# Kernel optimization log

Hardware: AMD Instinct MI355X
Metric: run time of the kernel (lower is better)

## Reference

```python
import jax, jax.numpy as jnp
import numpy as np

B, N, D, H = 2, 2048, 512, 8
HD = D // H
EPS = 1e-5


def layernorm(x, g, b):
    m = jnp.mean(x, axis=-1, keepdims=True)
    v = jnp.var(x, axis=-1, keepdims=True)
    return (x - m) * jax.lax.rsqrt(v + EPS) * g + b


def setup_inputs() -> dict:
    key = jax.random.key(0)
    ks = jax.random.split(key, 16)
    s = 1.0 / np.sqrt(D)
    def lin(k, din, dout):
        k1, k2 = jax.random.split(k)
        return (jax.random.uniform(k1, (din, dout), jnp.float32, -s, s),
                jax.random.uniform(k2, (dout,), jnp.float32, -s, s))
    Wq, bq = lin(ks[0], D, D)
    Wk, bk = lin(ks[1], D, D)
    Wv, bv = lin(ks[2], D, D)
    Wo, bo = lin(ks[3], D, D)
    W1, b1 = lin(ks[4], D, 2 * D)
    W2, b2 = lin(ks[5], 2 * D, D)
    return {
        'y': jax.random.normal(ks[6], (B, N, D), jnp.float32),
        'Wq': Wq, 'bq': bq, 'Wk': Wk, 'bk': bk, 'Wv': Wv, 'bv': bv,
        'Wo': Wo, 'bo': bo,
        'ln1_g': jnp.ones((D,)), 'ln1_b': jnp.zeros((D,)),
        'ln2_g': jnp.ones((D,)), 'ln2_b': jnp.zeros((D,)),
        'W1': W1, 'b1': b1, 'W2': W2, 'b2': b2,
    }


def reference(y, Wq, bq, Wk, bk, Wv, bv, Wo, bo, ln1_g, ln1_b, ln2_g, ln2_b, W1, b1, W2, b2):
    x = layernorm(y, ln1_g, ln1_b)
    def heads(W, b):
        return (x @ W + b).reshape(B, N, H, HD).transpose(0, 2, 1, 3)  # bhnc
    q = heads(Wq, bq)
    k = heads(Wk, bk)
    v = heads(Wv, bv)
    score = jax.nn.softmax(jnp.einsum('bhic,bhjc->bhij', q, k) / np.sqrt(HD), axis=-1)
    r = jnp.einsum('bhij,bhjc->bhic', score, v)
    r = r.transpose(0, 2, 1, 3).reshape(B, N, D) @ Wo + bo
    y = y + r
    h = layernorm(y, ln2_g, ln2_b)
    h = jax.nn.gelu(h @ W1 + b1, approximate=False) @ W2 + b2
    return y + h
```

## Files before the change

kernel.cpp:

```cpp
#include <hip/hip_runtime.h>

#define DEVI __device__ __forceinline__

typedef unsigned short u16;
typedef unsigned int   u32;
typedef unsigned long long u64;
typedef float  f32x4  __attribute__((ext_vector_type(4)));
typedef __bf16 bf16x8 __attribute__((ext_vector_type(8)));

union FragU { bf16x8 b; u64 u[2]; __bf16 e[8]; };

DEVI u16 f2b(float x) { __bf16 t = (__bf16)x; return __builtin_bit_cast(u16, t); }

DEVI float exp2a(float x) { float r; asm("v_exp_f32 %0, %1" : "=v"(r) : "v"(x)); return r; }

DEVI void gload16(const void* g, void* l) {
  __builtin_amdgcn_global_load_lds((const __attribute__((address_space(1))) u32*)g,
                                   (__attribute__((address_space(3))) u32*)l, 16, 0, 0);
}

DEVI int swzo(int row, int kb) {
  return ((((kb >> 4) ^ row) & 7) << 4) | ((kb ^ row) & 8) | (kb & 7);
}

DEVI u64 ldswz(const char* base, int row, int kb) {
  return *reinterpret_cast<const u64*>(base + row * 128 + swzo(row, kb));
}

DEVI size_t gaddr(int row, int kbyte, int rowbytes) {
  return (size_t)row * rowbytes + (size_t)((kbyte & ~127) + swzo(row, kbyte & 127));
}

__global__ __launch_bounds__(256)
void transpose_all(const float* __restrict__ Wq, const float* __restrict__ Wk,
                   const float* __restrict__ Wv, const float* __restrict__ Wo,
                   const float* __restrict__ W1, const float* __restrict__ W2,
                   u16* __restrict__ wqkvT, u16* __restrict__ woT,
                   u16* __restrict__ w1T, u16* __restrict__ w2T) {
  __shared__ float tile[32][33];
  const int id = blockIdx.x;
  const float* src; u16* dst; int K, N, bx, by;
  if (id < 1024) {
    const int m = id >> 8, t = id & 255;
    K = 512; N = 512; bx = t & 15; by = t >> 4;
    src = (m == 0) ? Wq : (m == 1) ? Wk : (m == 2) ? Wv : Wo;
    dst = (m == 3) ? woT : wqkvT + m * 512 * 512;
  } else if (id < 1536) {
    const int t = id - 1024; K = 512; N = 1024; bx = t & 31; by = t >> 5;
    src = W1; dst = w1T;
  } else {
    const int t = id - 1536; K = 1024; N = 512; bx = t & 15; by = t >> 4;
    src = W2; dst = w2T;
  }
  const int tx = threadIdx.x & 31, ty = threadIdx.x >> 5;
#pragma unroll
  for (int i = 0; i < 4; ++i)
    tile[ty + i * 8][tx] = src[(size_t)(by * 32 + ty + i * 8) * N + bx * 32 + tx];
  __syncthreads();
#pragma unroll
  for (int i = 0; i < 4; ++i) {
    const int n = bx * 32 + ty + i * 8;
    const int k = by * 32 + tx;
    *(u16*)((char*)dst + gaddr(n, 2 * k, 2 * K)) = f2b(tile[tx][ty + i * 8]);
  }
}

__global__ __launch_bounds__(256)
void ln_bf16(const float* __restrict__ x, const float* __restrict__ g,
             const float* __restrict__ b, char* __restrict__ out) {
  const int row = blockIdx.x;
  const int t = threadIdx.x;
  const float2 v = ((const float2*)(x + (size_t)row * 512))[t];
  float s1 = v.x + v.y, s2 = v.x * v.x + v.y * v.y;
#pragma unroll
  for (int off = 32; off; off >>= 1) { s1 += __shfl_xor(s1, off); s2 += __shfl_xor(s2, off); }
  __shared__ float a1[4], a2[4];
  const int w = t >> 6;
  if ((t & 63) == 0) { a1[w] = s1; a2[w] = s2; }
  __syncthreads();
  s1 = a1[0] + a1[1] + a1[2] + a1[3];
  s2 = a2[0] + a2[1] + a2[2] + a2[3];
  const float mean = s1 * (1.f / 512.f);
  const float var = s2 * (1.f / 512.f) - mean * mean;
  const float rstd = rsqrtf(var + 1e-5f);
  const float2 gg = ((const float2*)g)[t];
  const float2 bb = ((const float2*)b)[t];
  const u16 o0 = f2b((v.x - mean) * rstd * gg.x + bb.x);
  const u16 o1 = f2b((v.y - mean) * rstd * gg.y + bb.y);
  *(u32*)(out + gaddr(row, 4 * t, 1024)) = (u32)o0 | ((u32)o1 << 16);
}

enum { EPI_QKV = 0, EPI_RES = 1, EPI_GELU = 2 };

template <int EPI>
__global__ __launch_bounds__(256)
void gemm_bf16(const char* __restrict__ A, const char* __restrict__ Bt, int N, int K,
               const float* __restrict__ bias,
               const float* __restrict__ bq, const float* __restrict__ bk,
               const float* __restrict__ bv,
               const float* __restrict__ res, float* __restrict__ outF,
               char* __restrict__ outB,
               u16* __restrict__ qo, char* __restrict__ ko, char* __restrict__ vo) {
  __shared__ __align__(16) char sA[2][8192];
  __shared__ __align__(16) char sB[2][8192];
  const int tid = threadIdx.x;
  const int l = tid & 63, w = tid >> 6;
  const int tm = blockIdx.x, tn = blockIdx.y;
  const int wr = w >> 1, wc = w & 1;
  const int u = l >> 4, r16 = l & 15;
  const int lrow = l >> 3, lgr = l & 7;
  f32x4 acc[2][2] = {};
  const size_t KB = (size_t)K * 2;
  const char* Ab = A + (size_t)(tm * 64) * KB;
  const char* Bb = Bt + (size_t)(tn * 64) * KB;
  const int nkt = K >> 6;
  auto stage = [&](int buf, int kt) {
#pragma unroll
    for (int c = 0; c < 2; ++c) {
      const int chunk = w * 2 + c;
      const size_t off = (size_t)(chunk * 8 + lrow) * KB + (size_t)kt * 128 + (lgr << 4);
      gload16(Ab + off, sA[buf] + chunk * 1024);
      gload16(Bb + off, sB[buf] + chunk * 1024);
    }
  };
  stage(0, 0);
  int cur = 0;
  for (int kt = 0; kt < nkt; ++kt) {
    __syncthreads();
    if (kt + 1 < nkt) stage(cur ^ 1, kt + 1);
    __builtin_amdgcn_s_setprio(1);
#pragma unroll
    for (int ks = 0; ks < 2; ++ks) {
      FragU af[2], bfr[2];
      const int kb = ks * 64 + (u << 3);
#pragma unroll
      for (int i = 0; i < 2; ++i) {
        af[i].u[0]  = ldswz(sA[cur], wr * 32 + i * 16 + r16, kb);
        af[i].u[1]  = ldswz(sA[cur], wr * 32 + i * 16 + r16, kb + 32);
        bfr[i].u[0] = ldswz(sB[cur], wc * 32 + i * 16 + r16, kb);
        bfr[i].u[1] = ldswz(sB[cur], wc * 32 + i * 16 + r16, kb + 32);
      }
#pragma unroll
      for (int mi = 0; mi < 2; ++mi)
#pragma unroll
        for (int ni = 0; ni < 2; ++ni)
          acc[mi][ni] = __builtin_amdgcn_mfma_f32_16x16x32_bf16(af[mi].b, bfr[ni].b,
                                                                acc[mi][ni], 0, 0, 0);
    }
    __builtin_amdgcn_s_setprio(0);
    cur ^= 1;
  }
  const int row0 = tm * 64 + wr * 32 + (u << 2);
  const int col0 = tn * 64 + wc * 32 + r16;
#pragma unroll
  for (int mi = 0; mi < 2; ++mi) {
#pragma unroll
    for (int ni = 0; ni < 2; ++ni) {
      const int col = col0 + ni * 16;
      if (EPI == EPI_RES) {
#pragma unroll
        for (int r = 0; r < 4; ++r) {
          const int row = row0 + mi * 16 + r;
          outF[(size_t)row * N + col] = acc[mi][ni][r] + bias[col] + res[(size_t)row * N + col];
        }
      } else if (EPI == EPI_GELU) {
#pragma unroll
        for (int r = 0; r < 4; ++r) {
          const int row = row0 + mi * 16 + r;
          const float x = acc[mi][ni][r] + bias[col];
          *(u16*)(outB + gaddr(row, 2 * col, 2 * N)) =
              f2b(0.5f * x * (1.f + erff(x * 0.70710678118f)));
        }
      } else {
        const int which = col >> 9, cc = col & 511;
        const int h = cc >> 6, hd = cc & 63;
        if (which == 2) {
          const int rowa = row0 + mi * 16;
          const int bb2 = rowa >> 11, nt0 = rowa & 2047;
          const int bh = bb2 * 8 + h;
          const float bvv = bv[cc];
          union { ushort4 s; u64 q; } pk;
          pk.s.x = f2b(acc[mi][ni][0] + bvv);
          pk.s.y = f2b(acc[mi][ni][1] + bvv);
          pk.s.z = f2b(acc[mi][ni][2] + bvv);
          pk.s.w = f2b(acc[mi][ni][3] + bvv);
          *(u64*)(vo + (size_t)bh * 262144 + (size_t)(nt0 >> 6) * 8192 +
                  gaddr(hd, 2 * (nt0 & 63), 128)) = pk.q;
        } else {
#pragma unroll
          for (int r = 0; r < 4; ++r) {
            const int row = row0 + mi * 16 + r;
            const int bb2 = row >> 11, nt = row & 2047;
            const int bh = bb2 * 8 + h;
            if (which == 0)
              qo[((size_t)bh * 2048 + nt) * 64 + hd] = f2b((acc[mi][ni][r] + bq[cc]) * 0.18033688f);
            else
              *(u16*)(ko + (size_t)bh * 262144 + (size_t)(nt >> 6) * 8192 +
                      gaddr(nt & 63, 2 * hd, 128)) = f2b(acc[mi][ni][r] + bk[cc]);
          }
        }
      }
    }
  }
}

__global__ __launch_bounds__(512)
void attn_k(const u16* __restrict__ q, const char* __restrict__ kswz,
            const char* __restrict__ vswz, char* __restrict__ r_out) {
  __shared__ __align__(16) char sK[2][2][8192];
  __shared__ __align__(16) char sV[2][2][8192];
  const int tid = threadIdx.x;
  const int l = tid & 63, w = tid >> 6;
  const int kvh = w & 1, qw = w >> 1;
  const int bh = blockIdx.x, qt = blockIdx.y;
  const int u = l >> 4, r16 = l & 15;
  const char* kp = kswz + (size_t)bh * 262144;
  const char* vp = vswz + (size_t)bh * 262144;
  const int c0 = qw * 2;
  auto stage = [&](int buf, int t) {
#pragma unroll
    for (int c = 0; c < 2; ++c) {
      gload16(kp + (size_t)t * 8192 + (c0 + c) * 1024 + l * 16, sK[kvh][buf] + (c0 + c) * 1024);
      gload16(vp + (size_t)t * 8192 + (c0 + c) * 1024 + l * 16, sV[kvh][buf] + (c0 + c) * 1024);
    }
  };
  stage(0, kvh * 16);
  FragU qf[2];
  {
    const u16* qr = q + (size_t)bh * (2048 * 64) + (size_t)(qt * 64 + qw * 16 + r16) * 64 + (u << 2);
    qf[0].u[0] = *(const u64*)qr;        qf[0].u[1] = *(const u64*)(qr + 16);
    qf[1].u[0] = *(const u64*)(qr + 32); qf[1].u[1] = *(const u64*)(qr + 48);
  }
  float mrun = -1e30f, lrun = 0.f;
  f32x4 o[4] = {};
  int cur = 0;
  for (int i = 0; i < 16; ++i) {
    __syncthreads();
    if (i < 15) stage(cur ^ 1, kvh * 16 + i + 1);
    f32x4 st[4] = {};
    __builtin_amdgcn_s_setprio(1);
#pragma unroll
    for (int ks = 0; ks < 2; ++ks) {
      const int kb = ks * 64 + (u << 3);
#pragma unroll
      for (int mi = 0; mi < 4; ++mi) {
        FragU kf;
        kf.u[0] = ldswz(sK[kvh][cur], mi * 16 + r16, kb);
        kf.u[1] = ldswz(sK[kvh][cur], mi * 16 + r16, kb + 32);
        st[mi] = __builtin_amdgcn_mfma_f32_16x16x32_bf16(kf.b, qf[ks].b, st[mi], 0, 0, 0);
      }
    }
    __builtin_amdgcn_s_setprio(0);
    float tmax = -1e30f;
#pragma unroll
    for (int mi = 0; mi < 4; ++mi)
#pragma unroll
      for (int r = 0; r < 4; ++r) tmax = fmaxf(tmax, st[mi][r]);
    tmax = fmaxf(tmax, __shfl_xor(tmax, 16));
    tmax = fmaxf(tmax, __shfl_xor(tmax, 32));
    if (!__all(tmax <= mrun + 11.5f)) {
      const float mnew = fmaxf(mrun, tmax);
      const float alpha = exp2a(mrun - mnew);
      lrun *= alpha;
#pragma unroll
      for (int mo = 0; mo < 4; ++mo) o[mo] *= alpha;
      mrun = mnew;
    }
    float p[4][4];
    float tsum = 0.f;
#pragma unroll
    for (int mi = 0; mi < 4; ++mi)
#pragma unroll
      for (int r = 0; r < 4; ++r) { p[mi][r] = exp2a(st[mi][r] - mrun); tsum += p[mi][r]; }
    tsum += __shfl_xor(tsum, 16);
    tsum += __shfl_xor(tsum, 32);
    lrun += tsum;
    FragU pb[2];
#pragma unroll
    for (int ks = 0; ks < 2; ++ks)
#pragma unroll
      for (int j = 0; j < 4; ++j) {
        pb[ks].e[j]     = (__bf16)p[2 * ks][j];
        pb[ks].e[j + 4] = (__bf16)p[2 * ks + 1][j];
      }
    __builtin_amdgcn_s_setprio(1);
#pragma unroll
    for (int ks = 0; ks < 2; ++ks) {
      const int kb = ks * 64 + (u << 3);
#pragma unroll
      for (int mo = 0; mo < 4; ++mo) {
        FragU vf;
        vf.u[0] = ldswz(sV[kvh][cur], mo * 16 + r16, kb);
        vf.u[1] = ldswz(sV[kvh][cur], mo * 16 + r16, kb + 32);
        o[mo] = __builtin_amdgcn_mfma_f32_16x16x32_bf16(vf.b, pb[ks].b, o[mo], 0, 0, 0);
      }
    }
    __builtin_amdgcn_s_setprio(0);
    cur ^= 1;
  }
  __syncthreads();
  float* scrO  = (float*)&sK[0][0][0];
  float* scrML = (float*)&sV[0][0][0];
  if (kvh == 1) {
    if (u == 0) { scrML[qw * 32 + r16] = mrun; scrML[qw * 32 + 16 + r16] = lrun; }
#pragma unroll
    for (int mo = 0; mo < 4; ++mo)
#pragma unroll
      for (int r = 0; r < 4; ++r)
        scrO[qw * 1024 + (mo * 16 + u * 4 + r) * 16 + r16] = o[mo][r];
  }
  __syncthreads();
  if (kvh == 0) {
    const float m1 = scrML[qw * 32 + r16], l1 = scrML[qw * 32 + 16 + r16];
    const float m = fmaxf(mrun, m1);
    const float a0 = exp2a(mrun - m), a1 = exp2a(m1 - m);
    const float linv = 1.f / (lrun * a0 + l1 * a1);
    const float f0 = a0 * linv, f1 = a1 * linv;
    const int tok = (bh >> 3) * 2048 + qt * 64 + qw * 16 + r16;
    const int h = bh & 7;
#pragma unroll
    for (int mo = 0; mo < 4; ++mo) {
      union { ushort4 s; u64 qq; } pk;
      float vv[4];
#pragma unroll
      for (int r = 0; r < 4; ++r)
        vv[r] = o[mo][r] * f0 + scrO[qw * 1024 + (mo * 16 + u * 4 + r) * 16 + r16] * f1;
      pk.s.x = f2b(vv[0]); pk.s.y = f2b(vv[1]); pk.s.z = f2b(vv[2]); pk.s.w = f2b(vv[3]);
      *(u64*)(r_out + (size_t)tok * 1024 + h * 128 + swzo(tok, mo * 32 + (u << 3))) = pk.qq;
    }
  }
}

extern "C" void kernel_launch(void* const* d_in, const int* in_sizes, int n_in,
                              void* d_out, int out_size, void* d_ws, size_t ws_size,
                              hipStream_t stream) {
  const float* y    = (const float*)d_in[0];
  const float* Wq   = (const float*)d_in[1];
  const float* bq   = (const float*)d_in[2];
  const float* Wk   = (const float*)d_in[3];
  const float* bk   = (const float*)d_in[4];
  const float* Wv   = (const float*)d_in[5];
  const float* bv   = (const float*)d_in[6];
  const float* Wo   = (const float*)d_in[7];
  const float* bo   = (const float*)d_in[8];
  const float* ln1g = (const float*)d_in[9];
  const float* ln1b = (const float*)d_in[10];
  const float* ln2g = (const float*)d_in[11];
  const float* ln2b = (const float*)d_in[12];
  const float* W1   = (const float*)d_in[13];
  const float* b1   = (const float*)d_in[14];
  const float* W2   = (const float*)d_in[15];
  const float* b2   = (const float*)d_in[16];
  float* out = (float*)d_out;
  char* ws = (char*)d_ws;
  char* xb    = ws;
  u16*  qb    = (u16*)(ws + (4u << 20));
  char* kswz  = ws + (8u << 20);
  char* vswz  = ws + (12u << 20);
  char* rb    = ws + (16u << 20);
  char* g1b   = ws + (20u << 20);
  u16* wqkvT  = (u16*)(ws + (28u << 20));
  u16* woT    = wqkvT + 1536 * 512;
  u16* w1T    = woT + 512 * 512;
  u16* w2T    = w1T + 1024 * 512;

  transpose_all<<<2048, 256, 0, stream>>>(Wq, Wk, Wv, Wo, W1, W2, wqkvT, woT, w1T, w2T);
  ln_bf16<<<4096, 256, 0, stream>>>(y, ln1g, ln1b, xb);
  gemm_bf16<EPI_QKV><<<dim3(64, 24), 256, 0, stream>>>(
      xb, (const char*)wqkvT, 1536, 512, nullptr, bq, bk, bv,
      nullptr, nullptr, nullptr, qb, kswz, vswz);
  attn_k<<<dim3(16, 32), 512, 0, stream>>>(qb, kswz, vswz, rb);
  gemm_bf16<EPI_RES><<<dim3(64, 8), 256, 0, stream>>>(
      rb, (const char*)woT, 512, 512, bo, nullptr, nullptr, nullptr,
      y, out, nullptr, nullptr, nullptr, nullptr);
  ln_bf16<<<4096, 256, 0, stream>>>(out, ln2g, ln2b, xb);
  gemm_bf16<EPI_GELU><<<dim3(64, 16), 256, 0, stream>>>(
      xb, (const char*)w1T, 1024, 512, b1, nullptr, nullptr, nullptr,
      nullptr, nullptr, g1b, nullptr, nullptr, nullptr);
  gemm_bf16<EPI_RES><<<dim3(64, 8), 256, 0, stream>>>(
      g1b, (const char*)w2T, 512, 1024, b2, nullptr, nullptr, nullptr,
      out, out, nullptr, nullptr, nullptr, nullptr);
}
```

Measured before the change: 111.5 us.

## Enlarge GEMM tiles to 64x64 per wave and fuse weight transpose with first layernorm

The GEMM kernel is templated on the warp grid, and each wave now computes a 64x64 output tile with 4x4 MFMA fragments instead of 32x32. This gives blocks of 128x128 or 64x128, raising data reuse per LDS load and cutting block counts. The weight transpose and the first layernorm are merged into a single launch to save one kernel launch. The larger register footprint may lower occupancy, and the smaller grids (e.g. 256 blocks for the output projections) may underfill the 256 CUs.

```diff
diff --git a/kernel.cpp b/kernel.cpp
--- a/kernel.cpp
+++ b/kernel.cpp
@@ -32,36 +32,61 @@
 }
 
 __global__ __launch_bounds__(256)
-void transpose_all(const float* __restrict__ Wq, const float* __restrict__ Wk,
-                   const float* __restrict__ Wv, const float* __restrict__ Wo,
-                   const float* __restrict__ W1, const float* __restrict__ W2,
-                   u16* __restrict__ wqkvT, u16* __restrict__ woT,
-                   u16* __restrict__ w1T, u16* __restrict__ w2T) {
-  __shared__ float tile[32][33];
+void prep(const float* __restrict__ Wq, const float* __restrict__ Wk,
+          const float* __restrict__ Wv, const float* __restrict__ Wo,
+          const float* __restrict__ W1, const float* __restrict__ W2,
+          u16* __restrict__ wqkvT, u16* __restrict__ woT,
+          u16* __restrict__ w1T, u16* __restrict__ w2T,
+          const float* __restrict__ y, const float* __restrict__ ln1g,
+          const float* __restrict__ ln1b, char* __restrict__ xb) {
   const int id = blockIdx.x;
-  const float* src; u16* dst; int K, N, bx, by;
-  if (id < 1024) {
-    const int m = id >> 8, t = id & 255;
-    K = 512; N = 512; bx = t & 15; by = t >> 4;
-    src = (m == 0) ? Wq : (m == 1) ? Wk : (m == 2) ? Wv : Wo;
-    dst = (m == 3) ? woT : wqkvT + m * 512 * 512;
-  } else if (id < 1536) {
-    const int t = id - 1024; K = 512; N = 1024; bx = t & 31; by = t >> 5;
-    src = W1; dst = w1T;
+  if (id < 2048) {
+    __shared__ float tile[32][33];
+    const float* src; u16* dst; int K, N, bx, by;
+    if (id < 1024) {
+      const int m = id >> 8, t = id & 255;
+      K = 512; N = 512; bx = t & 15; by = t >> 4;
+      src = (m == 0) ? Wq : (m == 1) ? Wk : (m == 2) ? Wv : Wo;
+      dst = (m == 3) ? woT : wqkvT + m * 512 * 512;
+    } else if (id < 1536) {
+      const int t = id - 1024; K = 512; N = 1024; bx = t & 31; by = t >> 5;
+      src = W1; dst = w1T;
+    } else {
+      const int t = id - 1536; K = 1024; N = 512; bx = t & 15; by = t >> 4;
+      src = W2; dst = w2T;
+    }
+    const int tx = threadIdx.x & 31, ty = threadIdx.x >> 5;
+#pragma unroll
+    for (int i = 0; i < 4; ++i)
+      tile[ty + i * 8][tx] = src[(size_t)(by * 32 + ty + i * 8) * N + bx * 32 + tx];
+    __syncthreads();
+#pragma unroll
+    for (int i = 0; i < 4; ++i) {
+      const int n = bx * 32 + ty + i * 8;
+      const int k = by * 32 + tx;
+      *(u16*)((char*)dst + gaddr(n, 2 * k, 2 * K)) = f2b(tile[tx][ty + i * 8]);
+    }
   } else {
-    const int t = id - 1536; K = 1024; N = 512; bx = t & 15; by = t >> 4;
-    src = W2; dst = w2T;
-  }
-  const int tx = threadIdx.x & 31, ty = threadIdx.x >> 5;
-#pragma unroll
-  for (int i = 0; i < 4; ++i)
-    tile[ty + i * 8][tx] = src[(size_t)(by * 32 + ty + i * 8) * N + bx * 32 + tx];
-  __syncthreads();
-#pragma unroll
-  for (int i = 0; i < 4; ++i) {
-    const int n = bx * 32 + ty + i * 8;
-    const int k = by * 32 + tx;
-    *(u16*)((char*)dst + gaddr(n, 2 * k, 2 * K)) = f2b(tile[tx][ty + i * 8]);
+    const int row = id - 2048;
+    const int t = threadIdx.x;
+    const float2 v = ((const float2*)(y + (size_t)row * 512))[t];
+    float s1 = v.x + v.y, s2 = v.x * v.x + v.y * v.y;
+#pragma unroll
+    for (int off = 32; off; off >>= 1) { s1 += __shfl_xor(s1, off); s2 += __shfl_xor(s2, off); }
+    __shared__ float a1[4], a2[4];
+    const int w = t >> 6;
+    if ((t & 63) == 0) { a1[w] = s1; a2[w] = s2; }
+    __syncthreads();
+    s1 = a1[0] + a1[1] + a1[2] + a1[3];
+    s2 = a2[0] + a2[1] + a2[2] + a2[3];
+    const float mean = s1 * (1.f / 512.f);
+    const float var = s2 * (1.f / 512.f) - mean * mean;
+    const float rstd = rsqrtf(var + 1e-5f);
+    const float2 gg = ((const float2*)ln1g)[t];
+    const float2 bb = ((const float2*)ln1b)[t];
+    const u16 o0 = f2b((v.x - mean) * rstd * gg.x + bb.x);
+    const u16 o1 = f2b((v.y - mean) * rstd * gg.y + bb.y);
+    *(u32*)(xb + gaddr(row, 4 * t, 1024)) = (u32)o0 | ((u32)o1 << 16);
   }
 }
 
@@ -92,8 +117,8 @@
 
 enum { EPI_QKV = 0, EPI_RES = 1, EPI_GELU = 2 };
 
-template <int EPI>
-__global__ __launch_bounds__(256)
+template <int EPI, int WM, int WN>
+__global__ __launch_bounds__(WM * WN * 64)
 void gemm_bf16(const char* __restrict__ A, const char* __restrict__ Bt, int N, int K,
                const float* __restrict__ bias,
                const float* __restrict__ bq, const float* __restrict__ bk,
@@ -101,26 +126,32 @@
                const float* __restrict__ res, float* __restrict__ outF,
                char* __restrict__ outB,
                u16* __restrict__ qo, char* __restrict__ ko, char* __restrict__ vo) {
-  __shared__ __align__(16) char sA[2][8192];
-  __shared__ __align__(16) char sB[2][8192];
+  constexpr int NW = WM * WN, TM = WM * 64, TN = WN * 64;
+  constexpr int NCH = (WM + WN) * 8;
+  __shared__ __align__(16) char sA[2][TM * 128];
+  __shared__ __align__(16) char sB[2][TN * 128];
   const int tid = threadIdx.x;
   const int l = tid & 63, w = tid >> 6;
   const int tm = blockIdx.x, tn = blockIdx.y;
-  const int wr = w >> 1, wc = w & 1;
+  const int wr = w / WN, wc = w % WN;
   const int u = l >> 4, r16 = l & 15;
   const int lrow = l >> 3, lgr = l & 7;
-  f32x4 acc[2][2] = {};
+  f32x4 acc[4][4] = {};
   const size_t KB = (size_t)K * 2;
-  const char* Ab = A + (size_t)(tm * 64) * KB;
-  const char* Bb = Bt + (size_t)(tn * 64) * KB;
+  const char* Ab = A + (size_t)(tm * TM) * KB;
+  const char* Bb = Bt + (size_t)(tn * TN) * KB;
   const int nkt = K >> 6;
   auto stage = [&](int buf, int kt) {
 #pragma unroll
-    for (int c = 0; c < 2; ++c) {
-      const int chunk = w * 2 + c;
-      const size_t off = (size_t)(chunk * 8 + lrow) * KB + (size_t)kt * 128 + (lgr << 4);
-      gload16(Ab + off, sA[buf] + chunk * 1024);
-      gload16(Bb + off, sB[buf] + chunk * 1024);
+    for (int c = w; c < NCH; c += NW) {
+      if (c < WM * 8) {
+        gload16(Ab + (size_t)(c * 8 + lrow) * KB + (size_t)kt * 128 + (lgr << 4),
+                sA[buf] + c * 1024);
+      } else {
+        const int c2 = c - WM * 8;
+        gload16(Bb + (size_t)(c2 * 8 + lrow) * KB + (size_t)kt * 128 + (lgr << 4),
+                sB[buf] + c2 * 1024);
+      }
     }
   };
   stage(0, 0);
@@ -131,31 +162,31 @@
     __builtin_amdgcn_s_setprio(1);
 #pragma unroll
     for (int ks = 0; ks < 2; ++ks) {
-      FragU af[2], bfr[2];
+      FragU af[4], bfr[4];
       const int kb = ks * 64 + (u << 3);
 #pragma unroll
-      for (int i = 0; i < 2; ++i) {
-        af[i].u[0]  = ldswz(sA[cur], wr * 32 + i * 16 + r16, kb);
-        af[i].u[1]  = ldswz(sA[cur], wr * 32 + i * 16 + r16, kb + 32);
-        bfr[i].u[0] = ldswz(sB[cur], wc * 32 + i * 16 + r16, kb);
-        bfr[i].u[1] = ldswz(sB[cur], wc * 32 + i * 16 + r16, kb + 32);
-      }
-#pragma unroll
-      for (int mi = 0; mi < 2; ++mi)
-#pragma unroll
-        for (int ni = 0; ni < 2; ++ni)
+      for (int i = 0; i < 4; ++i) {
+        af[i].u[0]  = ldswz(sA[cur], wr * 64 + i * 16 + r16, kb);
+        af[i].u[1]  = ldswz(sA[cur], wr * 64 + i * 16 + r16, kb + 32);
+        bfr[i].u[0] = ldswz(sB[cur], wc * 64 + i * 16 + r16, kb);
+        bfr[i].u[1] = ldswz(sB[cur], wc * 64 + i * 16 + r16, kb + 32);
+      }
+#pragma unroll
+      for (int mi = 0; mi < 4; ++mi)
+#pragma unroll
+        for (int ni = 0; ni < 4; ++ni)
           acc[mi][ni] = __builtin_amdgcn_mfma_f32_16x16x32_bf16(af[mi].b, bfr[ni].b,
                                                                 acc[mi][ni], 0, 0, 0);
     }
     __builtin_amdgcn_s_setprio(0);
     cur ^= 1;
   }
-  const int row0 = tm * 64 + wr * 32 + (u << 2);
-  const int col0 = tn * 64 + wc * 32 + r16;
-#pragma unroll
-  for (int mi = 0; mi < 2; ++mi) {
-#pragma unroll
-    for (int ni = 0; ni < 2; ++ni) {
+  const int row0 = tm * TM + wr * 64 + (u << 2);
+  const int col0 = tn * TN + wc * 64 + r16;
+#pragma unroll
+  for (int mi = 0; mi < 4; ++mi) {
+#pragma unroll
+    for (int ni = 0; ni < 4; ++ni) {
       const int col = col0 + ni * 16;
       if (EPI == EPI_RES) {
 #pragma unroll
@@ -364,20 +395,20 @@
   u16* w1T    = woT + 512 * 512;
   u16* w2T    = w1T + 1024 * 512;
 
-  transpose_all<<<2048, 256, 0, stream>>>(Wq, Wk, Wv, Wo, W1, W2, wqkvT, woT, w1T, w2T);
-  ln_bf16<<<4096, 256, 0, stream>>>(y, ln1g, ln1b, xb);
-  gemm_bf16<EPI_QKV><<<dim3(64, 24), 256, 0, stream>>>(
+  prep<<<6144, 256, 0, stream>>>(Wq, Wk, Wv, Wo, W1, W2, wqkvT, woT, w1T, w2T,
+                                 y, ln1g, ln1b, xb);
+  gemm_bf16<EPI_QKV, 2, 2><<<dim3(32, 12), 256, 0, stream>>>(
       xb, (const char*)wqkvT, 1536, 512, nullptr, bq, bk, bv,
       nullptr, nullptr, nullptr, qb, kswz, vswz);
   attn_k<<<dim3(16, 32), 512, 0, stream>>>(qb, kswz, vswz, rb);
-  gemm_bf16<EPI_RES><<<dim3(64, 8), 256, 0, stream>>>(
+  gemm_bf16<EPI_RES, 1, 2><<<dim3(64, 4), 128, 0, stream>>>(
       rb, (const char*)woT, 512, 512, bo, nullptr, nullptr, nullptr,
       y, out, nullptr, nullptr, nullptr, nullptr);
   ln_bf16<<<4096, 256, 0, stream>>>(out, ln2g, ln2b, xb);
-  gemm_bf16<EPI_GELU><<<dim3(64, 16), 256, 0, stream>>>(
+  gemm_bf16<EPI_GELU, 2, 2><<<dim3(32, 8), 256, 0, stream>>>(
       xb, (const char*)w1T, 1024, 512, b1, nullptr, nullptr, nullptr,
       nullptr, nullptr, g1b, nullptr, nullptr, nullptr);
-  gemm_bf16<EPI_RES><<<dim3(64, 8), 256, 0, stream>>>(
+  gemm_bf16<EPI_RES, 1, 2><<<dim3(64, 4), 128, 0, stream>>>(
       g1b, (const char*)w2T, 512, 1024, b2, nullptr, nullptr, nullptr,
       out, out, nullptr, nullptr, nullptr, nullptr);
 }
```

Result: slower. 136.0 us (+22.0%).
